# Optimization experiments

Measured on AMD Instinct MI355X. Metric: run time of the kernel, lower is better.

Reference implementation:

```python
import jax, jax.numpy as jnp
import numpy as np

N_HEAD = 16
N_EMBD = 64  # per-head dim in this module's convention
INNER = N_HEAD * N_EMBD  # 1024


def setup_inputs() -> dict:
    key = jax.random.key(0)
    ks = jax.random.split(key, 6)
    B, S = 4, 2048
    scale = 0.02
    return {
        "x": jax.random.normal(ks[0], (B, S, N_EMBD), dtype=jnp.float32),
        "Wq": jax.random.normal(ks[1], (N_EMBD, INNER), dtype=jnp.float32) * scale,
        "Wk": jax.random.normal(ks[2], (N_EMBD, INNER), dtype=jnp.float32) * scale,
        "Wv": jax.random.normal(ks[3], (N_EMBD, INNER), dtype=jnp.float32) * scale,
        "Wo": jax.random.normal(ks[4], (INNER, N_EMBD), dtype=jnp.float32) * scale,
        "bo": jax.random.normal(ks[5], (N_EMBD,), dtype=jnp.float32) * scale,
        "causal_mask": 1,
    }


def reference(x, Wq, Wk, Wv, Wo, bo, causal_mask):
    B, S, _ = x.shape
    # projections: [B,S,INNER] -> [B,H,S,D]
    def split_heads(t):
        return t.reshape(B, S, N_HEAD, N_EMBD).transpose(0, 2, 1, 3)
    q = split_heads(x @ Wq)
    k = split_heads(x @ Wk)
    v = split_heads(x @ Wv)
    # [B,H,S,S]
    scores = jnp.einsum("bhqd,bhkd->bhqk", q, k) / jnp.sqrt(jnp.float32(N_EMBD))
    if causal_mask:
        future = jnp.triu(jnp.ones((S, S), dtype=scores.dtype), k=1)
        scores = scores - 1e9 * future  # matches torch: subtract 1e9*mask
    attn = jax.nn.softmax(scores, axis=-1)
    out = jnp.einsum("bhqk,bhkd->bhqd", attn, v)
    out = out.transpose(0, 2, 1, 3).reshape(B, S, INNER)
    return out @ Wo + bo
```

## Files before the change

### kernel.cpp

```cpp
#include <hip/hip_runtime.h>
#include <hip/hip_bf16.h>

#define NHEAD 16
#define HDIM 64
#define DINNER 1024
#define NBATCH 4
#define SEQ 2048
#define NTOK (NBATCH*SEQ)

typedef __bf16 bf16;
typedef __bf16 bf16x4 __attribute__((ext_vector_type(4)));
typedef __bf16 bf16x8 __attribute__((ext_vector_type(8)));
typedef float f32x4 __attribute__((ext_vector_type(4)));

#define OFF_BO   8
#define OFF_XB   128
#define OFF_WQT  (OFF_XB + NTOK*HDIM)
#define OFF_WKT  (OFF_WQT + DINNER*HDIM)
#define OFF_WVT  (OFF_WKT + DINNER*HDIM)
#define OFF_WOT  (OFF_WVT + DINNER*HDIM)
#define OFF_Q    (OFF_WOT + DINNER*HDIM)
#define OFF_K    (OFF_Q + NTOK*DINNER)
#define OFF_VT   (OFF_K + NTOK*DINNER)
#define OFF_ATT  (OFF_VT + NTOK*DINNER)

#define SSCALE 0.18033688011112042f
#define MASKVAL (-3.0e8f)
#define EOFF 2.0f

static __device__ __forceinline__ bf16x8 ld8(const bf16* p) {
  return *reinterpret_cast<const bf16x8*>(p);
}

static __device__ __forceinline__ int detect_isbf(const void* x, int tid,
                                                  int* sflag) {
  if (tid < 64) {
    const unsigned short* xb = (const unsigned short*)x;
    bool ok = true;
#pragma unroll
    for (int i = 0; i < 8; i++) {
      unsigned e = (xb[tid * 8 + i] >> 7) & 0xFF;
      ok = ok && (e >= 64 && e <= 140);
    }
    unsigned long long mball = __ballot(ok);
    if (tid == 0) *sflag = (mball == ~0ull) ? 1 : 0;
  }
  __syncthreads();
  return *sflag;
}

__global__ __launch_bounds__(256) void prep_kernel(
    const void* __restrict__ x, const void* __restrict__ Wq,
    const void* __restrict__ Wk, const void* __restrict__ Wv,
    const void* __restrict__ Wo, const void* __restrict__ bo,
    bf16* __restrict__ ws) {
  __shared__ int sflag;
  int isbf = detect_isbf(x, threadIdx.x, &sflag);
  int z = blockIdx.y;
  int idx = blockIdx.x * 256 + threadIdx.x;
  if (z < 3) {
    const void* src = (z == 0) ? Wq : (z == 1) ? Wk : Wv;
    bf16* dst = ws + ((z == 0) ? OFF_WQT : (z == 1) ? OFF_WKT : OFF_WVT);
    int n = idx >> 6, d = idx & 63;
    int i = d * DINNER + n;
    dst[n * HDIM + d] = isbf ? ((const bf16*)src)[i] : (bf16)((const float*)src)[i];
  } else if (z == 3) {
    int n = idx >> 10, k = idx & 1023;
    int i = k * HDIM + n;
    ws[OFF_WOT + n * DINNER + k] = isbf ? ((const bf16*)Wo)[i] : (bf16)((const float*)Wo)[i];
  } else if (z == 4) {
    int i = idx * 8;
    bf16x8 v;
    if (isbf) {
      v = ld8((const bf16*)x + i);
    } else {
      f32x4 a = *reinterpret_cast<const f32x4*>((const float*)x + i);
      f32x4 b2 = *reinterpret_cast<const f32x4*>((const float*)x + i + 4);
#pragma unroll
      for (int j = 0; j < 4; j++) { v[j] = (bf16)a[j]; v[4 + j] = (bf16)b2[j]; }
    }
    *reinterpret_cast<bf16x8*>(&ws[OFF_XB + i]) = v;
  } else {
    if (idx < 64) ws[OFF_BO + idx] = isbf ? ((const bf16*)bo)[idx] : (bf16)((const float*)bo)[idx];
  }
}

__global__ __launch_bounds__(256) void qkv_kernel(bf16* __restrict__ ws) {
  int tt = blockIdx.x, pz = blockIdx.z;
  int nc = blockIdx.y * 4 + (threadIdx.x >> 6);
  int lane = threadIdx.x & 63;
  int lq = lane & 15, quad = lane >> 4;
  const bf16* WT = ws + OFF_WQT + pz * (DINNER * HDIM);
  int n0 = nc * 64;
  bf16x8 w0[4], w1[4];
#pragma unroll
  for (int c = 0; c < 4; c++) {
    const bf16* wr = WT + (n0 + c * 16 + lq) * HDIM;
    w0[c] = ld8(wr + quad * 8);
    w1[c] = ld8(wr + 32 + quad * 8);
  }
  bf16* Qb = ws + OFF_Q;
  bf16* Kb = ws + OFF_K;
  bf16* VTb = ws + OFF_VT;
#pragma unroll
  for (int mi = 0; mi < 4; mi++) {
    int t0 = tt * 64 + mi * 16;
    const bf16* xrow = ws + OFF_XB + (t0 + lq) * HDIM;
    bf16x8 x0 = ld8(xrow + quad * 8);
    bf16x8 x1 = ld8(xrow + 32 + quad * 8);
    int b = t0 >> 11, s0 = t0 & (SEQ - 1);
#pragma unroll
    for (int c = 0; c < 4; c++) {
      f32x4 z = {0.f, 0.f, 0.f, 0.f};
      z = __builtin_amdgcn_mfma_f32_16x16x32_bf16(w0[c], x0, z, 0, 0, 0);
      z = __builtin_amdgcn_mfma_f32_16x16x32_bf16(w1[c], x1, z, 0, 0, 0);
      if (pz < 2) {
        bf16x4 pk = {(bf16)z[0], (bf16)z[1], (bf16)z[2], (bf16)z[3]};
        bf16* P = (pz == 0) ? Qb : Kb;
        *reinterpret_cast<bf16x4*>(
            &P[((size_t)(b * NHEAD + nc) * SEQ + s0 + lq) * HDIM + c * 16 + quad * 4]) = pk;
      } else {
#pragma unroll
        for (int r = 0; r < 4; r++) {
          int d = c * 16 + quad * 4 + r;
          VTb[(((size_t)b * NHEAD + nc) * HDIM + d) * SEQ + s0 + lq] = (bf16)z[r];
        }
      }
    }
  }
}

__global__ __launch_bounds__(256, 2) void flash_kernel(const int* __restrict__ cmask,
                                                       bf16* __restrict__ ws) {
  __shared__ __align__(16) bf16 Kl[2][64 * 64];
  __shared__ __align__(16) bf16 Vl[2][64 * 64];
  __shared__ __align__(16) bf16 Pl[4][16 * 64];
  const int qmap[16] = {15,13,11,9,0,2,4,6,14,12,10,8,1,3,5,7};
  int bid = blockIdx.x;
  int bh = (bid & 7) * 8 + ((bid >> 3) & 7);
  int qt = qmap[bid >> 6];
  int w = threadIdx.x >> 6;
  int lane = threadIdx.x & 63;
  int lq = lane & 15, quad = lane >> 4;
  int causal = cmask[0];
  const bf16* Q = ws + OFF_Q + (size_t)bh * SEQ * HDIM;
  const bf16* K = ws + OFF_K + (size_t)bh * SEQ * HDIM;
  const bf16* VT = ws + OFF_VT + (size_t)bh * HDIM * SEQ;
  int b = bh >> 4, h = bh & 15;
  bf16* ar = ws + OFF_ATT;
  int sr = threadIdx.x >> 2;
  int sg = (threadIdx.x & 3) * 16;
  int sc0 = (((threadIdx.x & 3) * 2) ^ (sr & 7)) << 3;
  int sc1 = (((threadIdx.x & 3) * 2 + 1) ^ (sr & 7)) << 3;
  int rq0 = (quad ^ (lq & 7)) << 3;
  int rq1 = ((4 + quad) ^ (lq & 7)) << 3;

  int qb = qt * 128;
  int qw = qb + w * 32;
  int T = (causal ? (qb + 128) : SEQ) / 64;

  bf16x8 bq[2][2];
#pragma unroll
  for (int m = 0; m < 2; m++) {
    const bf16* qrow = Q + (qw + m * 16 + lq) * HDIM;
    bq[m][0] = ld8(qrow + quad * 8);
    bq[m][1] = ld8(qrow + 32 + quad * 8);
  }
  f32x4 o[2][4];
  float lsum[2] = {0.f, 0.f};
#pragma unroll
  for (int m = 0; m < 2; m++)
#pragma unroll
    for (int c = 0; c < 4; c++) o[m][c] = (f32x4){0.f, 0.f, 0.f, 0.f};

  bf16x8 kst0 = ld8(K + sr * HDIM + sg);
  bf16x8 kst1 = ld8(K + sr * HDIM + sg + 8);
  bf16x8 vst0 = ld8(VT + sr * SEQ + sg);
  bf16x8 vst1 = ld8(VT + sr * SEQ + sg + 8);

  for (int ti = 0; ti < T; ti++) {
    int buf = ti & 1;
    int k0 = ti * 64;
    *reinterpret_cast<bf16x8*>(&Kl[buf][sr * 64 + sc0]) = kst0;
    *reinterpret_cast<bf16x8*>(&Kl[buf][sr * 64 + sc1]) = kst1;
    *reinterpret_cast<bf16x8*>(&Vl[buf][sr * 64 + sc0]) = vst0;
    *reinterpret_cast<bf16x8*>(&Vl[buf][sr * 64 + sc1]) = vst1;
    int kn = (ti + 1 < T) ? (k0 + 64) : k0;
    kst0 = ld8(K + (kn + sr) * HDIM + sg);
    kst1 = ld8(K + (kn + sr) * HDIM + sg + 8);
    vst0 = ld8(VT + sr * SEQ + kn + sg);
    vst1 = ld8(VT + sr * SEQ + kn + sg + 8);
    __syncthreads();
    f32x4 st[2][4];
#pragma unroll
    for (int t = 0; t < 4; t++) {
      bf16x8 a0 = ld8(&Kl[buf][(t * 16 + lq) * 64 + rq0]);
      bf16x8 a1 = ld8(&Kl[buf][(t * 16 + lq) * 64 + rq1]);
#pragma unroll
      for (int m = 0; m < 2; m++) {
        f32x4 z = {0.f, 0.f, 0.f, 0.f};
        z = __builtin_amdgcn_mfma_f32_16x16x32_bf16(a0, bq[m][0], z, 0, 0, 0);
        z = __builtin_amdgcn_mfma_f32_16x16x32_bf16(a1, bq[m][1], z, 0, 0, 0);
        st[m][t] = z;
      }
    }
    bool needmask = causal && (k0 + 63 > qw);
    bf16x8 bp[2][2];
#pragma unroll
    for (int m = 0; m < 2; m++) {
      if (needmask) {
        int qrel = qw + m * 16 + lq - k0 - quad * 4;
#pragma unroll
        for (int t = 0; t < 4; t++)
#pragma unroll
          for (int r = 0; r < 4; r++)
            if (t * 16 + r > qrel) st[m][t][r] = MASKVAL;
      }
      float sum = 0.f;
#pragma unroll
      for (int t = 0; t < 4; t++) {
        float e0 = exp2f(fmaf(st[m][t][0], SSCALE, -EOFF));
        float e1 = exp2f(fmaf(st[m][t][1], SSCALE, -EOFF));
        float e2 = exp2f(fmaf(st[m][t][2], SSCALE, -EOFF));
        float e3 = exp2f(fmaf(st[m][t][3], SSCALE, -EOFF));
        sum += (e0 + e1) + (e2 + e3);
        bf16x4 pk = {(bf16)e0, (bf16)e1, (bf16)e2, (bf16)e3};
        int ch = ((t * 2 + (quad >> 1)) ^ (lq & 7)) << 3;
        *reinterpret_cast<bf16x4*>(&Pl[w][lq * 64 + ch + (quad & 1) * 4]) = pk;
      }
      lsum[m] += sum;
      bp[m][0] = ld8(&Pl[w][lq * 64 + rq0]);
      bp[m][1] = ld8(&Pl[w][lq * 64 + rq1]);
    }
#pragma unroll
    for (int c = 0; c < 4; c++) {
      bf16x8 av0 = ld8(&Vl[buf][(c * 16 + lq) * 64 + rq0]);
      bf16x8 av1 = ld8(&Vl[buf][(c * 16 + lq) * 64 + rq1]);
#pragma unroll
      for (int m = 0; m < 2; m++) {
        o[m][c] = __builtin_amdgcn_mfma_f32_16x16x32_bf16(av0, bp[m][0], o[m][c], 0, 0, 0);
        o[m][c] = __builtin_amdgcn_mfma_f32_16x16x32_bf16(av1, bp[m][1], o[m][c], 0, 0, 0);
      }
    }
  }
#pragma unroll
  for (int m = 0; m < 2; m++) {
    lsum[m] += __shfl_xor(lsum[m], 16);
    lsum[m] += __shfl_xor(lsum[m], 32);
    float inv = 1.0f / lsum[m];
    size_t rowoff = ((size_t)(b * SEQ + qw + m * 16 + lq)) * DINNER + h * HDIM;
#pragma unroll
    for (int c = 0; c < 4; c++) {
      bf16x4 ov = {(bf16)(o[m][c][0] * inv), (bf16)(o[m][c][1] * inv),
                   (bf16)(o[m][c][2] * inv), (bf16)(o[m][c][3] * inv)};
      *reinterpret_cast<bf16x4*>(&ar[rowoff + c * 16 + quad * 4]) = ov;
    }
  }
}

__global__ __launch_bounds__(256) void oproj_kernel(const bf16* __restrict__ ws,
                                                    const void* __restrict__ x,
                                                    void* __restrict__ outp) {
  __shared__ __align__(16) float red[3 * 64 * 16];
  __shared__ int sflag;
  int isbf = detect_isbf(x, threadIdx.x, &sflag);
  int tt = blockIdx.x;
  int w = threadIdx.x >> 6;
  int lane = threadIdx.x & 63;
  int lq = lane & 15, quad = lane >> 4;
  const bf16* A = ws + OFF_ATT + (size_t)(tt * 16 + lq) * DINNER;
  const bf16* WoT = ws + OFF_WOT;
  f32x4 acc[4];
#pragma unroll
  for (int c = 0; c < 4; c++) acc[c] = (f32x4){0.f, 0.f, 0.f, 0.f};
  int kbeg = w * 256;
  for (int k0 = kbeg; k0 < kbeg + 256; k0 += 32) {
    bf16x8 a = ld8(A + k0 + quad * 8);
#pragma unroll
    for (int c = 0; c < 4; c++) {
      bf16x8 b = ld8(WoT + (size_t)(c * 16 + lq) * DINNER + k0 + quad * 8);
      acc[c] = __builtin_amdgcn_mfma_f32_16x16x32_bf16(a, b, acc[c], 0, 0, 0);
    }
  }
  if (w > 0) {
#pragma unroll
    for (int c = 0; c < 4; c++)
      *reinterpret_cast<f32x4*>(&red[(((w - 1) * 64 + lane) * 4 + c) * 4]) = acc[c];
  }
  __syncthreads();
  if (w == 0) {
#pragma unroll
    for (int j = 0; j < 3; j++)
#pragma unroll
      for (int c = 0; c < 4; c++)
        acc[c] += *reinterpret_cast<f32x4*>(&red[((j * 64 + lane) * 4 + c) * 4]);
#pragma unroll
    for (int c = 0; c < 4; c++) {
      float bv = (float)ws[OFF_BO + c * 16 + lq];
#pragma unroll
      for (int r = 0; r < 4; r++) {
        int t = tt * 16 + quad * 4 + r;
        float v = acc[c][r] + bv;
        size_t oo = (size_t)t * HDIM + c * 16 + lq;
        if (isbf) ((bf16*)outp)[oo] = (bf16)v;
        else      ((float*)outp)[oo] = v;
      }
    }
  }
}

extern "C" void kernel_launch(void* const* d_in, const int* in_sizes, int n_in,
                              void* d_out, int out_size, void* d_ws, size_t ws_size,
                              hipStream_t stream) {
  const void* x  = d_in[0];
  const void* Wq = d_in[1];
  const void* Wk = d_in[2];
  const void* Wv = d_in[3];
  const void* Wo = d_in[4];
  const void* bo = d_in[5];
  const int* cm  = (const int*)d_in[6];
  bf16* ws = (bf16*)d_ws;

  hipLaunchKernelGGL(prep_kernel, dim3(256, 6), dim3(256), 0, stream,
                     x, Wq, Wk, Wv, Wo, bo, ws);
  hipLaunchKernelGGL(qkv_kernel, dim3(128, 4, 3), dim3(256), 0, stream, ws);
  hipLaunchKernelGGL(flash_kernel, dim3(1024), dim3(256), 0, stream, cm, ws);
  hipLaunchKernelGGL(oproj_kernel, dim3(512), dim3(256), 0, stream, ws, x, d_out);
}
```

Baseline: 168.3 us.

## Fold Wo into V projection and softmax scale into Wq, replace oproj with reduction

Each head's V is multiplied by that head's slice of Wo inside the QKV kernel, so attention directly produces per-head projected outputs and the final output projection shrinks to a bias-plus-sum over 16 heads. The softmax scale (with log2e) is folded into Wq during prep, which removes the per-element fma before exp2, and the prep transposes now read inputs coalesced. The mask value becomes -200 and the fixed exponent offset is dropped. Costs are an extra MFMA pass and an LDS round trip in the V path, plus extra bf16 rounding of the V·Wo product, and no max subtraction, which relies on scores staying small.

```diff
diff --git a/kernel.cpp b/kernel.cpp
--- a/kernel.cpp
+++ b/kernel.cpp
@@ -25,8 +25,6 @@
 #define OFF_ATT  (OFF_VT + NTOK*DINNER)
 
 #define SSCALE 0.18033688011112042f
-#define MASKVAL (-3.0e8f)
-#define EOFF 2.0f
 
 static __device__ __forceinline__ bf16x8 ld8(const bf16* p) {
   return *reinterpret_cast<const bf16x8*>(p);
@@ -61,13 +59,14 @@
   if (z < 3) {
     const void* src = (z == 0) ? Wq : (z == 1) ? Wk : Wv;
     bf16* dst = ws + ((z == 0) ? OFF_WQT : (z == 1) ? OFF_WKT : OFF_WVT);
-    int n = idx >> 6, d = idx & 63;
-    int i = d * DINNER + n;
-    dst[n * HDIM + d] = isbf ? ((const bf16*)src)[i] : (bf16)((const float*)src)[i];
+    int d = idx >> 10, n = idx & 1023;
+    float v = isbf ? (float)((const bf16*)src)[idx] : ((const float*)src)[idx];
+    if (z == 0) v *= SSCALE;
+    dst[n * HDIM + d] = (bf16)v;
   } else if (z == 3) {
-    int n = idx >> 10, k = idx & 1023;
-    int i = k * HDIM + n;
-    ws[OFF_WOT + n * DINNER + k] = isbf ? ((const bf16*)Wo)[i] : (bf16)((const float*)Wo)[i];
+    int k = idx >> 6, n = idx & 63;
+    float v = isbf ? (float)((const bf16*)Wo)[idx] : ((const float*)Wo)[idx];
+    ws[OFF_WOT + n * DINNER + k] = (bf16)v;
   } else if (z == 4) {
     int i = idx * 8;
     bf16x8 v;
@@ -86,8 +85,10 @@
 }
 
 __global__ __launch_bounds__(256) void qkv_kernel(bf16* __restrict__ ws) {
+  __shared__ __align__(16) bf16 Vst[4][16 * 72];
   int tt = blockIdx.x, pz = blockIdx.z;
-  int nc = blockIdx.y * 4 + (threadIdx.x >> 6);
+  int w = threadIdx.x >> 6;
+  int nc = blockIdx.y * 4 + w;
   int lane = threadIdx.x & 63;
   int lq = lane & 15, quad = lane >> 4;
   const bf16* WT = ws + OFF_WQT + pz * (DINNER * HDIM);
@@ -102,6 +103,16 @@
   bf16* Qb = ws + OFF_Q;
   bf16* Kb = ws + OFF_K;
   bf16* VTb = ws + OFF_VT;
+  bf16x8 ao0[4], ao1[4];
+  if (pz == 2) {
+    const bf16* WoT = ws + OFF_WOT;
+#pragma unroll
+    for (int c = 0; c < 4; c++) {
+      const bf16* orow = WoT + (size_t)(c * 16 + lq) * DINNER + nc * 64;
+      ao0[c] = ld8(orow + quad * 8);
+      ao1[c] = ld8(orow + 32 + quad * 8);
+    }
+  }
 #pragma unroll
   for (int mi = 0; mi < 4; mi++) {
     int t0 = tt * 64 + mi * 16;
@@ -109,21 +120,37 @@
     bf16x8 x0 = ld8(xrow + quad * 8);
     bf16x8 x1 = ld8(xrow + 32 + quad * 8);
     int b = t0 >> 11, s0 = t0 & (SEQ - 1);
-#pragma unroll
-    for (int c = 0; c < 4; c++) {
-      f32x4 z = {0.f, 0.f, 0.f, 0.f};
-      z = __builtin_amdgcn_mfma_f32_16x16x32_bf16(w0[c], x0, z, 0, 0, 0);
-      z = __builtin_amdgcn_mfma_f32_16x16x32_bf16(w1[c], x1, z, 0, 0, 0);
-      if (pz < 2) {
+    if (pz < 2) {
+#pragma unroll
+      for (int c = 0; c < 4; c++) {
+        f32x4 z = {0.f, 0.f, 0.f, 0.f};
+        z = __builtin_amdgcn_mfma_f32_16x16x32_bf16(w0[c], x0, z, 0, 0, 0);
+        z = __builtin_amdgcn_mfma_f32_16x16x32_bf16(w1[c], x1, z, 0, 0, 0);
         bf16x4 pk = {(bf16)z[0], (bf16)z[1], (bf16)z[2], (bf16)z[3]};
         bf16* P = (pz == 0) ? Qb : Kb;
         *reinterpret_cast<bf16x4*>(
             &P[((size_t)(b * NHEAD + nc) * SEQ + s0 + lq) * HDIM + c * 16 + quad * 4]) = pk;
-      } else {
+      }
+    } else {
+#pragma unroll
+      for (int c = 0; c < 4; c++) {
+        f32x4 z = {0.f, 0.f, 0.f, 0.f};
+        z = __builtin_amdgcn_mfma_f32_16x16x32_bf16(w0[c], x0, z, 0, 0, 0);
+        z = __builtin_amdgcn_mfma_f32_16x16x32_bf16(w1[c], x1, z, 0, 0, 0);
+        bf16x4 pk = {(bf16)z[0], (bf16)z[1], (bf16)z[2], (bf16)z[3]};
+        *reinterpret_cast<bf16x4*>(&Vst[w][lq * 72 + c * 16 + quad * 4]) = pk;
+      }
+      bf16x8 bv0 = ld8(&Vst[w][lq * 72 + quad * 8]);
+      bf16x8 bv1 = ld8(&Vst[w][lq * 72 + 32 + quad * 8]);
+#pragma unroll
+      for (int c = 0; c < 4; c++) {
+        f32x4 z2 = {0.f, 0.f, 0.f, 0.f};
+        z2 = __builtin_amdgcn_mfma_f32_16x16x32_bf16(ao0[c], bv0, z2, 0, 0, 0);
+        z2 = __builtin_amdgcn_mfma_f32_16x16x32_bf16(ao1[c], bv1, z2, 0, 0, 0);
 #pragma unroll
         for (int r = 0; r < 4; r++) {
           int d = c * 16 + quad * 4 + r;
-          VTb[(((size_t)b * NHEAD + nc) * HDIM + d) * SEQ + s0 + lq] = (bf16)z[r];
+          VTb[(((size_t)b * NHEAD + nc) * HDIM + d) * SEQ + s0 + lq] = (bf16)z2[r];
         }
       }
     }
@@ -214,15 +241,15 @@
         for (int t = 0; t < 4; t++)
 #pragma unroll
           for (int r = 0; r < 4; r++)
-            if (t * 16 + r > qrel) st[m][t][r] = MASKVAL;
+            if (t * 16 + r > qrel) st[m][t][r] = -200.0f;
       }
       float sum = 0.f;
 #pragma unroll
       for (int t = 0; t < 4; t++) {
-        float e0 = exp2f(fmaf(st[m][t][0], SSCALE, -EOFF));
-        float e1 = exp2f(fmaf(st[m][t][1], SSCALE, -EOFF));
-        float e2 = exp2f(fmaf(st[m][t][2], SSCALE, -EOFF));
-        float e3 = exp2f(fmaf(st[m][t][3], SSCALE, -EOFF));
+        float e0 = exp2f(st[m][t][0]);
+        float e1 = exp2f(st[m][t][1]);
+        float e2 = exp2f(st[m][t][2]);
+        float e3 = exp2f(st[m][t][3]);
         sum += (e0 + e1) + (e2 + e3);
         bf16x4 pk = {(bf16)e0, (bf16)e1, (bf16)e2, (bf16)e3};
         int ch = ((t * 2 + (quad >> 1)) ^ (lq & 7)) << 3;
@@ -258,55 +285,19 @@
   }
 }
 
-__global__ __launch_bounds__(256) void oproj_kernel(const bf16* __restrict__ ws,
-                                                    const void* __restrict__ x,
-                                                    void* __restrict__ outp) {
-  __shared__ __align__(16) float red[3 * 64 * 16];
+__global__ __launch_bounds__(256) void reduce_kernel(const bf16* __restrict__ ws,
+                                                     const void* __restrict__ x,
+                                                     void* __restrict__ outp) {
   __shared__ int sflag;
   int isbf = detect_isbf(x, threadIdx.x, &sflag);
-  int tt = blockIdx.x;
-  int w = threadIdx.x >> 6;
-  int lane = threadIdx.x & 63;
-  int lq = lane & 15, quad = lane >> 4;
-  const bf16* A = ws + OFF_ATT + (size_t)(tt * 16 + lq) * DINNER;
-  const bf16* WoT = ws + OFF_WOT;
-  f32x4 acc[4];
-#pragma unroll
-  for (int c = 0; c < 4; c++) acc[c] = (f32x4){0.f, 0.f, 0.f, 0.f};
-  int kbeg = w * 256;
-  for (int k0 = kbeg; k0 < kbeg + 256; k0 += 32) {
-    bf16x8 a = ld8(A + k0 + quad * 8);
-#pragma unroll
-    for (int c = 0; c < 4; c++) {
-      bf16x8 b = ld8(WoT + (size_t)(c * 16 + lq) * DINNER + k0 + quad * 8);
-      acc[c] = __builtin_amdgcn_mfma_f32_16x16x32_bf16(a, b, acc[c], 0, 0, 0);
-    }
-  }
-  if (w > 0) {
-#pragma unroll
-    for (int c = 0; c < 4; c++)
-      *reinterpret_cast<f32x4*>(&red[(((w - 1) * 64 + lane) * 4 + c) * 4]) = acc[c];
-  }
-  __syncthreads();
-  if (w == 0) {
-#pragma unroll
-    for (int j = 0; j < 3; j++)
-#pragma unroll
-      for (int c = 0; c < 4; c++)
-        acc[c] += *reinterpret_cast<f32x4*>(&red[((j * 64 + lane) * 4 + c) * 4]);
-#pragma unroll
-    for (int c = 0; c < 4; c++) {
-      float bv = (float)ws[OFF_BO + c * 16 + lq];
-#pragma unroll
-      for (int r = 0; r < 4; r++) {
-        int t = tt * 16 + quad * 4 + r;
-        float v = acc[c][r] + bv;
-        size_t oo = (size_t)t * HDIM + c * 16 + lq;
-        if (isbf) ((bf16*)outp)[oo] = (bf16)v;
-        else      ((float*)outp)[oo] = v;
-      }
-    }
-  }
+  int idx = blockIdx.x * 256 + threadIdx.x;
+  int t = idx >> 6, d = idx & 63;
+  const bf16* ar = ws + OFF_ATT + (size_t)t * DINNER + d;
+  float s = (float)ws[OFF_BO + d];
+#pragma unroll
+  for (int h = 0; h < 16; h++) s += (float)ar[h * 64];
+  if (isbf) ((bf16*)outp)[idx] = (bf16)s;
+  else      ((float*)outp)[idx] = s;
 }
 
 extern "C" void kernel_launch(void* const* d_in, const int* in_sizes, int n_in,
@@ -325,5 +316,5 @@
                      x, Wq, Wk, Wv, Wo, bo, ws);
   hipLaunchKernelGGL(qkv_kernel, dim3(128, 4, 3), dim3(256), 0, stream, ws);
   hipLaunchKernelGGL(flash_kernel, dim3(1024), dim3(256), 0, stream, cm, ws);
-  hipLaunchKernelGGL(oproj_kernel, dim3(512), dim3(256), 0, stream, ws, x, d_out);
-}
+  hipLaunchKernelGGL(reduce_kernel, dim3(2048), dim3(256), 0, stream, ws, x, d_out);
+}
```

Measured after the change: 161.2 us. -4.2%, faster.
